# Kernel optimization log

Hardware: AMD Instinct MI355X
Metric: run time of the kernel (lower is better)

## Reference

```python
import jax, jax.numpy as jnp
import numpy as np
from jax import lax

# Conv3d(in_dim, in_dim, kernel=(1,3,3), padding=(0,1,1)) == per-time-slice 3x3 conv mixing channels

def _conv3d(x, w, b):
    # x: [B, C, T, W, H], w: [O, I, 1, 3, 3], b: [O]
    y = lax.conv_general_dilated(
        x, w,
        window_strides=(1, 1, 1),
        padding=[(0, 0), (1, 1), (1, 1)],
        dimension_numbers=("NCDHW", "OIDHW", "NCDHW"),
    )
    return y + b[None, :, None, None, None]


def setup_inputs() -> dict:
    key = jax.random.key(0)
    ks = jax.random.split(key, 8)
    B, C, T, W, H = 8, 64, 16, 64, 64
    fan = C * 1 * 3 * 3
    bound = 1.0 / np.sqrt(fan)  # torch Conv3d default init range
    x = jax.random.normal(ks[0], (B, C, T, W, H), dtype=jnp.float32)
    wq = jax.random.uniform(ks[1], (C, C, 1, 3, 3), jnp.float32, -bound, bound)
    wk = jax.random.uniform(ks[2], (C, C, 1, 3, 3), jnp.float32, -bound, bound)
    wv = jax.random.uniform(ks[3], (C, C, 1, 3, 3), jnp.float32, -bound, bound)
    bq = jax.random.uniform(ks[4], (C,), jnp.float32, -bound, bound)
    bk = jax.random.uniform(ks[5], (C,), jnp.float32, -bound, bound)
    bv = jax.random.uniform(ks[6], (C,), jnp.float32, -bound, bound)
    # torch init is gamma=0 (identity output); use nonzero so reference exercises the full path
    gamma = jax.random.normal(ks[7], (1,), dtype=jnp.float32) * 0.1
    return {"x": x, "wq": wq, "wk": wk, "wv": wv,
            "bq": bq, "bk": bk, "bv": bv, "gamma": gamma}


def reference(x, wq, wk, wv, bq, bk, bv, gamma):
    B, C, T, W, H = x.shape
    WH = W * H
    q = _conv3d(x, wq, bq).reshape(B, C, T, WH)
    k = _conv3d(x, wk, bk).reshape(B, C, T, WH)
    v = _conv3d(x, wv, bv).reshape(B, C, T, WH)
    # Original: (q[...,:,None] @ k[...,None,:]) @ v[...,:,None]  -> rank-1 energy, no softmax.
    # Exact reassociation: out_i = q_i * sum_j(k_j * v_j), avoiding the [WH, WH] matrix.
    s = jnp.sum(k * v, axis=-1, keepdims=True)  # [B, C, T, 1]
    out = (q * s).reshape(B, C, T, W, H)
    return gamma[0] * out + x
```

## Files before the change

### kernel.cpp

```cpp
#include <hip/hip_runtime.h>
#include <hip/hip_bf16.h>
#include <stdint.h>

typedef __attribute__((ext_vector_type(8))) short bf16x8;
typedef __attribute__((ext_vector_type(4))) float f32x4v;
typedef __attribute__((ext_vector_type(16))) float f32x16;

#define CH_STRIDE 65536
#define ROW_B 8448
#define SLICE_B 557568

__device__ __forceinline__ uint16_t f2bf(float f) {
  uint32_t u = __builtin_bit_cast(uint32_t, f);
  u = (u + 0x7FFFu + ((u >> 16) & 1u)) >> 16;
  return (uint16_t)u;
}
__device__ __forceinline__ float bf2f(uint32_t b) {
  return __builtin_bit_cast(float, b << 16);
}
__device__ __forceinline__ uint16_t cvt_bf(float f) {
  return __builtin_bit_cast(uint16_t, __float2bfloat16(f));
}

#define MFMA32(a, b, c) __builtin_amdgcn_mfma_f32_32x32x16_bf16(a, b, c, 0, 0, 0)
#define WAIT0 asm volatile("s_waitcnt vmcnt(0) lgkmcnt(0)" ::: "memory")
#define BAR __builtin_amdgcn_s_barrier()
#define SCHED0 __builtin_amdgcn_sched_barrier(0)

#define LDSX6  (6 * 8 * 66 * 16)
#define LDSX10 (10 * 8 * 66 * 16)

__device__ __forceinline__ void gld16(const void* g, void* l) {
  __builtin_amdgcn_global_load_lds(
      (const __attribute__((address_space(1))) uint32_t*)g,
      (__attribute__((address_space(3))) uint32_t*)l, 16, 0, 0);
}

__device__ __forceinline__ bf16x8 ldx(const uint8_t* ldsx, int row, int oct, int ci) {
  return *(const bf16x8*)(ldsx + (uint32_t)((row * 8 + oct) * 66 + ci) * 16u);
}
__device__ __forceinline__ bf16x8 ldw_kv(const uint8_t* ldsw, int oct, int rowloc) {
  return *(const bf16x8*)(ldsw + (uint32_t)(oct * 128 + rowloc) * 16u);
}
__device__ __forceinline__ bf16x8 ldw_q(const uint8_t* ldsw, int oct, int row) {
  return *(const bf16x8*)(ldsw + (uint32_t)(oct * 64 + row) * 16u);
}

__global__ void prep_weights(const float* __restrict__ wq, const float* __restrict__ wk,
                             const float* __restrict__ wv, uint16_t* __restrict__ wout) {
  int i = blockIdx.x * 256 + threadIdx.x;
  if (i >= 110592) return;
  if (i < 36864) {
    int tap = i >> 12, oct = (i >> 9) & 7, row = (i >> 3) & 63, j = i & 7;
    wout[i] = f2bf(wq[(row * 64 + oct * 8 + j) * 9 + tap]);
  } else {
    int m = i - 36864;
    int tap = m >> 13, oct = (m >> 10) & 7, rl = (m >> 3) & 127, j = m & 7;
    const float* src = (rl < 64) ? wk : wv;
    wout[i] = f2bf(src[((rl & 63) * 64 + oct * 8 + j) * 9 + tap]);
  }
}

__global__ __launch_bounds__(256, 4) void transpose_x(const float* __restrict__ x,
                                                      uint8_t* __restrict__ xT) {
  const int tid = threadIdx.x;
  const int bid = blockIdx.x;
  const int gg = bid % 17, slice = bid / 17;
  const int b = slice >> 4, t = slice & 15;
  const int r0 = gg * 4;
  const int nrow = (gg == 16) ? 2 : 4;
  const float* xs = x + ((size_t)b * 1024 + t) * 4096;
  uint8_t* dst = xT + (size_t)slice * SLICE_B + (size_t)r0 * ROW_B;

  if (tid < nrow * 16) {
    int row = tid >> 4, rem = tid & 15;
    int oct = rem >> 1, side = rem & 1;
    bf16x8 z = {};
    *(bf16x8*)(dst + (uint32_t)((row * 8 + oct) * 66 + side * 65) * 16u) = z;
  }
  #pragma unroll
  for (int k = 0; k < 2; ++k) {
    int u = tid + k * 256;
    if (u < nrow * 128) {
      int row = u >> 7, oct = (u >> 4) & 7, g = u & 15;
      int w = r0 + row - 1;
      uint8_t* base = dst + (uint32_t)((row * 8 + oct) * 66 + 4 * g + 1) * 16u;
      if ((unsigned)w < 64u) {
        const float* p = xs + (size_t)(oct * 8) * CH_STRIDE + w * 64 + 4 * g;
        f32x4v v[8];
        #pragma unroll
        for (int j = 0; j < 8; ++j) v[j] = *(const f32x4v*)(p + (size_t)j * CH_STRIDE);
        #pragma unroll
        for (int c = 0; c < 4; ++c) {
          bf16x8 frag;
          #pragma unroll
          for (int q = 0; q < 4; ++q) {
            frag[2 * q]     = (short)cvt_bf(v[2 * q][c]);
            frag[2 * q + 1] = (short)cvt_bf(v[2 * q + 1][c]);
          }
          *(bf16x8*)(base + (uint32_t)c * 16u) = frag;
        }
      } else {
        bf16x8 z = {};
        #pragma unroll
        for (int c = 0; c < 4; ++c) *(bf16x8*)(base + (uint32_t)c * 16u) = z;
      }
    }
  }
}

__global__ __launch_bounds__(1024, 4) void kv_s_kernel(
    const uint8_t* __restrict__ xT, const uint16_t* __restrict__ wkv,
    const float* __restrict__ bk, const float* __restrict__ bv,
    float* __restrict__ s_out) {
  extern __shared__ uint8_t lds[];
  uint8_t* ldsx = lds;
  uint8_t* ldswA = lds + LDSX10;
  uint8_t* ldswB = lds + LDSX10 + 16384;
  const int tid = threadIdx.x;
  const int l = tid & 63;
  const int wid = tid >> 6;
  const int ng = wid & 7, mg = wid >> 3;
  int bid = (int)(blockIdx.x & 7) * 128 + (int)(blockIdx.x >> 3);
  const int rg = bid & 7, slice = bid >> 3;
  const int b = slice >> 4, t = slice & 15;
  const int w0 = rg * 8;
  const int lm = l & 31, lh = l >> 5;

  const uint8_t* gx = xT + (size_t)slice * SLICE_B + (size_t)w0 * ROW_B;
  #pragma unroll
  for (int k = 0; k < 6; ++k) {
    int idx = tid + k * 1024;
    if (idx < 5280) gld16(gx + (uint32_t)idx * 16u, ldsx + (uint32_t)idx * 16u);
  }
  gld16(wkv + (size_t)tid * 8, ldswA + (uint32_t)tid * 16u);
  SCHED0; WAIT0; BAR; SCHED0;

  f32x16 accK[2], accV[2];
  #pragma unroll
  for (int nt = 0; nt < 2; ++nt)
    #pragma unroll
    for (int q = 0; q < 16; ++q) { accK[nt][q] = 0.f; accV[nt][q] = 0.f; }

  #pragma unroll
  for (int tap = 0; tap < 9; ++tap) {
    const int dy = tap / 3, dx = tap % 3;
    const uint8_t* bufc = (tap & 1) ? ldswB : ldswA;
    uint8_t* bufn = (tap & 1) ? ldswA : ldswB;
    if (tap < 8)
      gld16(wkv + ((size_t)(tap + 1) * 1024 + tid) * 8, bufn + (uint32_t)tid * 16u);
    __builtin_amdgcn_s_setprio(1);
    #pragma unroll
    for (int s = 0; s < 4; ++s) {
      int oct = s * 2 + lh;
      bf16x8 aK = ldw_kv(bufc, oct, mg * 32 + lm);
      bf16x8 aV = ldw_kv(bufc, oct, 64 + mg * 32 + lm);
      bf16x8 b0 = ldx(ldsx, ng + dy, oct, lm + dx);
      bf16x8 b1 = ldx(ldsx, ng + dy, oct, 32 + lm + dx);
      accK[0] = MFMA32(aK, b0, accK[0]);
      accK[1] = MFMA32(aK, b1, accK[1]);
      accV[0] = MFMA32(aV, b0, accV[0]);
      accV[1] = MFMA32(aV, b1, accV[1]);
    }
    __builtin_amdgcn_s_setprio(0);
    SCHED0; WAIT0; BAR; SCHED0;
  }

  __syncthreads();
  float* red = (float*)lds;
  #pragma unroll
  for (int q = 0; q < 16; ++q) {
    int cl = (q & 3) + 8 * (q >> 2) + 4 * lh;
    int c = mg * 32 + cl;
    float bkc = bk[c], bvc = bv[c];
    float p = (accK[0][q] + bkc) * (accV[0][q] + bvc)
            + (accK[1][q] + bkc) * (accV[1][q] + bvc);
    red[c * 261 + ng * 32 + lm] = p;
  }
  __syncthreads();
  if (tid < 64) {
    const float* rp = red + tid * 261;
    f32x4v a4 = {0.f, 0.f, 0.f, 0.f};
    #pragma unroll
    for (int j = 0; j < 64; ++j) a4 += *(const f32x4v*)(rp + j * 4);
    atomicAdd(s_out + (b * 16 + t) * 64 + tid, a4[0] + a4[1] + a4[2] + a4[3]);
  }
}

__global__ __launch_bounds__(256, 2) void q_out_kernel(
    const uint8_t* __restrict__ xT, const uint16_t* __restrict__ wq,
    const float* __restrict__ bq, const float* __restrict__ s_in,
    const float* __restrict__ gamma, float* __restrict__ out) {
  extern __shared__ uint8_t lds[];
  uint8_t* ldsx = lds;
  uint8_t* ldswA = lds + LDSX6;
  uint8_t* ldswB = lds + LDSX6 + 8192;
  const int tid = threadIdx.x;
  const int l = tid & 63, ng = tid >> 6;
  int bid = (int)(blockIdx.x & 7) * 256 + (int)(blockIdx.x >> 3);
  const int rg = bid & 15, slice = bid >> 4;
  const int b = slice >> 4, t = slice & 15;
  const int w0 = rg * 4;
  const int lm = l & 31, lh = l >> 5;

  const uint8_t* gx = xT + (size_t)slice * SLICE_B + (size_t)w0 * ROW_B;
  #pragma unroll
  for (int k = 0; k < 13; ++k) {
    int idx = tid + k * 256;
    if (idx < 3168) gld16(gx + (uint32_t)idx * 16u, ldsx + (uint32_t)idx * 16u);
  }
  #pragma unroll
  for (int k = 0; k < 2; ++k)
    gld16(wq + (size_t)(tid + k * 256) * 8, ldswA + (uint32_t)(tid + k * 256) * 16u);
  SCHED0; WAIT0; BAR; SCHED0;

  f32x16 acc[2][2];
  #pragma unroll
  for (int mt = 0; mt < 2; ++mt)
    #pragma unroll
    for (int nt = 0; nt < 2; ++nt)
      #pragma unroll
      for (int q = 0; q < 16; ++q) acc[mt][nt][q] = 0.f;

  #pragma unroll
  for (int tap = 0; tap < 9; ++tap) {
    const int dy = tap / 3, dx = tap % 3;
    const uint8_t* bufc = (tap & 1) ? ldswB : ldswA;
    uint8_t* bufn = (tap & 1) ? ldswA : ldswB;
    if (tap < 8) {
      #pragma unroll
      for (int k = 0; k < 2; ++k)
        gld16(wq + ((size_t)(tap + 1) * 512 + tid + k * 256) * 8,
              bufn + (uint32_t)(tid + k * 256) * 16u);
    }
    __builtin_amdgcn_s_setprio(1);
    #pragma unroll
    for (int s = 0; s < 4; ++s) {
      int oct = s * 2 + lh;
      bf16x8 a0 = ldw_q(bufc, oct, lm);
      bf16x8 a1 = ldw_q(bufc, oct, 32 + lm);
      bf16x8 b0 = ldx(ldsx, ng + dy, oct, lm + dx);
      bf16x8 b1 = ldx(ldsx, ng + dy, oct, 32 + lm + dx);
      acc[0][0] = MFMA32(a0, b0, acc[0][0]);
      acc[0][1] = MFMA32(a0, b1, acc[0][1]);
      acc[1][0] = MFMA32(a1, b0, acc[1][0]);
      acc[1][1] = MFMA32(a1, b1, acc[1][1]);
    }
    __builtin_amdgcn_s_setprio(0);
    SCHED0; WAIT0; BAR; SCHED0;
  }

  float g = gamma[0];
  const float* sb = s_in + (b * 16 + t) * 64;
  int w = w0 + ng;
  #pragma unroll
  for (int mt = 0; mt < 2; ++mt) {
    #pragma unroll
    for (int q = 0; q < 16; ++q) {
      int cl = (q & 3) + 8 * (q >> 2) + 4 * lh;
      int c  = mt * 32 + cl;
      float qb = bq[c], sc = sb[c];
      #pragma unroll
      for (int nt = 0; nt < 2; ++nt) {
        int h = nt * 32 + lm;
        uint32_t xb = (uint32_t)(((ng + 1) * 8 + (c >> 3)) * 66 + (h + 1)) * 16u
                    + (uint32_t)(c & 7) * 2u;
        float xv = bf2f(*(const uint16_t*)(ldsx + xb));
        size_t idx = ((size_t)(b * 64 + c) * 16 + t) * 4096 + (size_t)w * 64 + h;
        out[idx] = g * (acc[mt][nt][q] + qb) * sc + xv;
      }
    }
  }
}

extern "C" void kernel_launch(void* const* d_in, const int* in_sizes, int n_in,
                              void* d_out, int out_size, void* d_ws, size_t ws_size,
                              hipStream_t stream) {
  const float* x   = (const float*)d_in[0];
  const float* wq  = (const float*)d_in[1];
  const float* wk  = (const float*)d_in[2];
  const float* wv  = (const float*)d_in[3];
  const float* bq  = (const float*)d_in[4];
  const float* bk  = (const float*)d_in[5];
  const float* bv  = (const float*)d_in[6];
  const float* gam = (const float*)d_in[7];

  uint16_t* wbf = (uint16_t*)d_ws;
  float* sbuf   = (float*)((uint8_t*)d_ws + 221184);
  uint8_t* xT   = (uint8_t*)d_ws + 1048576;
  if (ws_size < (size_t)1048576 + 128 * (size_t)SLICE_B) return;

  hipMemsetAsync(sbuf, 0, 8 * 16 * 64 * sizeof(float), stream);
  prep_weights<<<(110592 + 255) / 256, 256, 0, stream>>>(wq, wk, wv, wbf);
  transpose_x<<<128 * 17, 256, 0, stream>>>(x, xT);
  kv_s_kernel<<<1024, 1024, LDSX10 + 32768, stream>>>(xT, wbf + 36864, bk, bv, sbuf);
  q_out_kernel<<<2048, 256, LDSX6 + 16384, stream>>>(xT, wbf, bq, sbuf, gam, (float*)d_out);
}
```

Baseline: 180.2 us.

## Fuse x transpose/bf16 conversion into conv kernels, drop intermediate xT buffer

New measurement: 153.2 us. -15.0%, faster.

```diff
diff --git a/kernel.cpp b/kernel.cpp
--- a/kernel.cpp
+++ b/kernel.cpp
@@ -7,8 +7,6 @@
 typedef __attribute__((ext_vector_type(16))) float f32x16;
 
 #define CH_STRIDE 65536
-#define ROW_B 8448
-#define SLICE_B 557568
 
 __device__ __forceinline__ uint16_t f2bf(float f) {
   uint32_t u = __builtin_bit_cast(uint32_t, f);
@@ -44,6 +42,40 @@
 }
 __device__ __forceinline__ bf16x8 ldw_q(const uint8_t* ldsw, int oct, int row) {
   return *(const bf16x8*)(ldsw + (uint32_t)(oct * 64 + row) * 16u);
+}
+
+__device__ __forceinline__ void stage_unit(uint8_t* ldsx, const float* xs, int w0, int u) {
+  int row = u >> 7, oct = (u >> 4) & 7, g = u & 15;
+  int w = w0 - 1 + row;
+  uint32_t base = (uint32_t)((row * 8 + oct) * 66 + 4 * g + 1) * 16u;
+  if ((unsigned)w < 64u) {
+    const float* p = xs + (size_t)(oct * 8) * CH_STRIDE + w * 64 + 4 * g;
+    f32x4v v[8];
+    #pragma unroll
+    for (int j = 0; j < 8; ++j) v[j] = *(const f32x4v*)(p + (size_t)j * CH_STRIDE);
+    #pragma unroll
+    for (int c = 0; c < 4; ++c) {
+      bf16x8 frag;
+      #pragma unroll
+      for (int q = 0; q < 4; ++q) {
+        frag[2 * q]     = (short)cvt_bf(v[2 * q][c]);
+        frag[2 * q + 1] = (short)cvt_bf(v[2 * q + 1][c]);
+      }
+      *(bf16x8*)(ldsx + base + (uint32_t)c * 16u) = frag;
+    }
+  } else {
+    bf16x8 z = {};
+    #pragma unroll
+    for (int c = 0; c < 4; ++c) *(bf16x8*)(ldsx + base + (uint32_t)c * 16u) = z;
+  }
+}
+__device__ __forceinline__ void stage_halo(uint8_t* ldsx, int tid, int nrow) {
+  if (tid < nrow * 16) {
+    int row = tid >> 4, rem = tid & 15;
+    int oct = rem >> 1, side = rem & 1;
+    bf16x8 z = {};
+    *(bf16x8*)(ldsx + (uint32_t)((row * 8 + oct) * 66 + side * 65) * 16u) = z;
+  }
 }
 
 __global__ void prep_weights(const float* __restrict__ wq, const float* __restrict__ wk,
@@ -61,56 +93,8 @@
   }
 }
 
-__global__ __launch_bounds__(256, 4) void transpose_x(const float* __restrict__ x,
-                                                      uint8_t* __restrict__ xT) {
-  const int tid = threadIdx.x;
-  const int bid = blockIdx.x;
-  const int gg = bid % 17, slice = bid / 17;
-  const int b = slice >> 4, t = slice & 15;
-  const int r0 = gg * 4;
-  const int nrow = (gg == 16) ? 2 : 4;
-  const float* xs = x + ((size_t)b * 1024 + t) * 4096;
-  uint8_t* dst = xT + (size_t)slice * SLICE_B + (size_t)r0 * ROW_B;
-
-  if (tid < nrow * 16) {
-    int row = tid >> 4, rem = tid & 15;
-    int oct = rem >> 1, side = rem & 1;
-    bf16x8 z = {};
-    *(bf16x8*)(dst + (uint32_t)((row * 8 + oct) * 66 + side * 65) * 16u) = z;
-  }
-  #pragma unroll
-  for (int k = 0; k < 2; ++k) {
-    int u = tid + k * 256;
-    if (u < nrow * 128) {
-      int row = u >> 7, oct = (u >> 4) & 7, g = u & 15;
-      int w = r0 + row - 1;
-      uint8_t* base = dst + (uint32_t)((row * 8 + oct) * 66 + 4 * g + 1) * 16u;
-      if ((unsigned)w < 64u) {
-        const float* p = xs + (size_t)(oct * 8) * CH_STRIDE + w * 64 + 4 * g;
-        f32x4v v[8];
-        #pragma unroll
-        for (int j = 0; j < 8; ++j) v[j] = *(const f32x4v*)(p + (size_t)j * CH_STRIDE);
-        #pragma unroll
-        for (int c = 0; c < 4; ++c) {
-          bf16x8 frag;
-          #pragma unroll
-          for (int q = 0; q < 4; ++q) {
-            frag[2 * q]     = (short)cvt_bf(v[2 * q][c]);
-            frag[2 * q + 1] = (short)cvt_bf(v[2 * q + 1][c]);
-          }
-          *(bf16x8*)(base + (uint32_t)c * 16u) = frag;
-        }
-      } else {
-        bf16x8 z = {};
-        #pragma unroll
-        for (int c = 0; c < 4; ++c) *(bf16x8*)(base + (uint32_t)c * 16u) = z;
-      }
-    }
-  }
-}
-
-__global__ __launch_bounds__(1024, 4) void kv_s_kernel(
-    const uint8_t* __restrict__ xT, const uint16_t* __restrict__ wkv,
+__global__ __launch_bounds__(512, 2) void kv_s_kernel(
+    const float* __restrict__ x, const uint16_t* __restrict__ wkv,
     const float* __restrict__ bk, const float* __restrict__ bv,
     float* __restrict__ s_out) {
   extern __shared__ uint8_t lds[];
@@ -119,48 +103,60 @@
   uint8_t* ldswB = lds + LDSX10 + 16384;
   const int tid = threadIdx.x;
   const int l = tid & 63;
-  const int wid = tid >> 6;
-  const int ng = wid & 7, mg = wid >> 3;
+  const int ng = tid >> 6;
   int bid = (int)(blockIdx.x & 7) * 128 + (int)(blockIdx.x >> 3);
   const int rg = bid & 7, slice = bid >> 3;
   const int b = slice >> 4, t = slice & 15;
   const int w0 = rg * 8;
+  const float* xs = x + ((size_t)b * 1024 + t) * 4096;
   const int lm = l & 31, lh = l >> 5;
 
-  const uint8_t* gx = xT + (size_t)slice * SLICE_B + (size_t)w0 * ROW_B;
-  #pragma unroll
-  for (int k = 0; k < 6; ++k) {
-    int idx = tid + k * 1024;
-    if (idx < 5280) gld16(gx + (uint32_t)idx * 16u, ldsx + (uint32_t)idx * 16u);
-  }
   gld16(wkv + (size_t)tid * 8, ldswA + (uint32_t)tid * 16u);
+  gld16(wkv + (size_t)(tid + 512) * 8, ldswA + (uint32_t)(tid + 512) * 16u);
+  stage_halo(ldsx, tid, 10);
+  #pragma unroll
+  for (int k = 0; k < 3; ++k) {
+    int u = tid + k * 512;
+    if (u < 1280) stage_unit(ldsx, xs, w0, u);
+  }
   SCHED0; WAIT0; BAR; SCHED0;
 
-  f32x16 accK[2], accV[2];
-  #pragma unroll
-  for (int nt = 0; nt < 2; ++nt)
-    #pragma unroll
-    for (int q = 0; q < 16; ++q) { accK[nt][q] = 0.f; accV[nt][q] = 0.f; }
+  f32x16 accK[2][2], accV[2][2];
+  #pragma unroll
+  for (int mt = 0; mt < 2; ++mt)
+    #pragma unroll
+    for (int nt = 0; nt < 2; ++nt)
+      #pragma unroll
+      for (int q = 0; q < 16; ++q) { accK[mt][nt][q] = 0.f; accV[mt][nt][q] = 0.f; }
 
   #pragma unroll
   for (int tap = 0; tap < 9; ++tap) {
     const int dy = tap / 3, dx = tap % 3;
     const uint8_t* bufc = (tap & 1) ? ldswB : ldswA;
     uint8_t* bufn = (tap & 1) ? ldswA : ldswB;
-    if (tap < 8)
+    if (tap < 8) {
       gld16(wkv + ((size_t)(tap + 1) * 1024 + tid) * 8, bufn + (uint32_t)tid * 16u);
+      gld16(wkv + ((size_t)(tap + 1) * 1024 + tid + 512) * 8,
+            bufn + (uint32_t)(tid + 512) * 16u);
+    }
     __builtin_amdgcn_s_setprio(1);
     #pragma unroll
     for (int s = 0; s < 4; ++s) {
       int oct = s * 2 + lh;
-      bf16x8 aK = ldw_kv(bufc, oct, mg * 32 + lm);
-      bf16x8 aV = ldw_kv(bufc, oct, 64 + mg * 32 + lm);
-      bf16x8 b0 = ldx(ldsx, ng + dy, oct, lm + dx);
-      bf16x8 b1 = ldx(ldsx, ng + dy, oct, 32 + lm + dx);
-      accK[0] = MFMA32(aK, b0, accK[0]);
-      accK[1] = MFMA32(aK, b1, accK[1]);
-      accV[0] = MFMA32(aV, b0, accV[0]);
-      accV[1] = MFMA32(aV, b1, accV[1]);
+      bf16x8 aK0 = ldw_kv(bufc, oct, lm);
+      bf16x8 aK1 = ldw_kv(bufc, oct, 32 + lm);
+      bf16x8 aV0 = ldw_kv(bufc, oct, 64 + lm);
+      bf16x8 aV1 = ldw_kv(bufc, oct, 96 + lm);
+      bf16x8 b0  = ldx(ldsx, ng + dy, oct, lm + dx);
+      bf16x8 b1  = ldx(ldsx, ng + dy, oct, 32 + lm + dx);
+      accK[0][0] = MFMA32(aK0, b0, accK[0][0]);
+      accK[0][1] = MFMA32(aK0, b1, accK[0][1]);
+      accK[1][0] = MFMA32(aK1, b0, accK[1][0]);
+      accK[1][1] = MFMA32(aK1, b1, accK[1][1]);
+      accV[0][0] = MFMA32(aV0, b0, accV[0][0]);
+      accV[0][1] = MFMA32(aV0, b1, accV[0][1]);
+      accV[1][0] = MFMA32(aV1, b0, accV[1][0]);
+      accV[1][1] = MFMA32(aV1, b1, accV[1][1]);
     }
     __builtin_amdgcn_s_setprio(0);
     SCHED0; WAIT0; BAR; SCHED0;
@@ -171,11 +167,14 @@
   #pragma unroll
   for (int q = 0; q < 16; ++q) {
     int cl = (q & 3) + 8 * (q >> 2) + 4 * lh;
-    int c = mg * 32 + cl;
-    float bkc = bk[c], bvc = bv[c];
-    float p = (accK[0][q] + bkc) * (accV[0][q] + bvc)
-            + (accK[1][q] + bkc) * (accV[1][q] + bvc);
-    red[c * 261 + ng * 32 + lm] = p;
+    #pragma unroll
+    for (int mt = 0; mt < 2; ++mt) {
+      int c = mt * 32 + cl;
+      float bkc = bk[c], bvc = bv[c];
+      float p = (accK[mt][0][q] + bkc) * (accV[mt][0][q] + bvc)
+              + (accK[mt][1][q] + bkc) * (accV[mt][1][q] + bvc);
+      red[c * 261 + ng * 32 + lm] = p;
+    }
   }
   __syncthreads();
   if (tid < 64) {
@@ -188,7 +187,7 @@
 }
 
 __global__ __launch_bounds__(256, 2) void q_out_kernel(
-    const uint8_t* __restrict__ xT, const uint16_t* __restrict__ wq,
+    const float* __restrict__ x, const uint16_t* __restrict__ wq,
     const float* __restrict__ bq, const float* __restrict__ s_in,
     const float* __restrict__ gamma, float* __restrict__ out) {
   extern __shared__ uint8_t lds[];
@@ -201,17 +200,15 @@
   const int rg = bid & 15, slice = bid >> 4;
   const int b = slice >> 4, t = slice & 15;
   const int w0 = rg * 4;
+  const float* xs = x + ((size_t)b * 1024 + t) * 4096;
   const int lm = l & 31, lh = l >> 5;
 
-  const uint8_t* gx = xT + (size_t)slice * SLICE_B + (size_t)w0 * ROW_B;
-  #pragma unroll
-  for (int k = 0; k < 13; ++k) {
-    int idx = tid + k * 256;
-    if (idx < 3168) gld16(gx + (uint32_t)idx * 16u, ldsx + (uint32_t)idx * 16u);
-  }
   #pragma unroll
   for (int k = 0; k < 2; ++k)
     gld16(wq + (size_t)(tid + k * 256) * 8, ldswA + (uint32_t)(tid + k * 256) * 16u);
+  stage_halo(ldsx, tid, 6);
+  #pragma unroll
+  for (int k = 0; k < 3; ++k) stage_unit(ldsx, xs, w0, tid + k * 256);
   SCHED0; WAIT0; BAR; SCHED0;
 
   f32x16 acc[2][2];
@@ -287,12 +284,9 @@
 
   uint16_t* wbf = (uint16_t*)d_ws;
   float* sbuf   = (float*)((uint8_t*)d_ws + 221184);
-  uint8_t* xT   = (uint8_t*)d_ws + 1048576;
-  if (ws_size < (size_t)1048576 + 128 * (size_t)SLICE_B) return;
 
   hipMemsetAsync(sbuf, 0, 8 * 16 * 64 * sizeof(float), stream);
   prep_weights<<<(110592 + 255) / 256, 256, 0, stream>>>(wq, wk, wv, wbf);
-  transpose_x<<<128 * 17, 256, 0, stream>>>(x, xT);
-  kv_s_kernel<<<1024, 1024, LDSX10 + 32768, stream>>>(xT, wbf + 36864, bk, bv, sbuf);
-  q_out_kernel<<<2048, 256, LDSX6 + 16384, stream>>>(xT, wbf, bq, sbuf, gam, (float*)d_out);
-}
+  kv_s_kernel<<<1024, 512, LDSX10 + 32768, stream>>>(x, wbf + 36864, bk, bv, sbuf);
+  q_out_kernel<<<2048, 256, LDSX6 + 16384, stream>>>(x, wbf, bq, sbuf, gam, (float*)d_out);
+}
```
